# Performance work log

Hardware: AMD Instinct MI355X
Metric: run time of the kernel (lower is better)

## Reference

```python
import jax, jax.numpy as jnp
import numpy as np

# ---- module hyperparameters (match init_kwargs) ----
N_BASIS = 4            # lagrange polynomial order n
SEGMENTS = 32
IN_CHANNELS = 64
LENGTH = 2.0
HALF = 0.5 * LENGTH
W_WIDTH = (N_BASIS - 1) * SEGMENTS + 1  # 97
# Lagrange interpolation nodes on [-HALF, HALF] (uniform, as in high_order_layers_torch LagrangePoly)
_XNODES = np.linspace(-HALF, HALF, N_BASIS).astype(np.float32)


def _lagrange_basis(x):
    """x: [...] -> basis values [..., n]; basis_j(x) = prod_{m!=j} (x-X_m)/(X_j-X_m)."""
    X = jnp.asarray(_XNODES, dtype=x.dtype)
    eye = jnp.eye(N_BASIS, dtype=bool)
    denom = jnp.where(eye, 1.0, X[:, None] - X[None, :])          # [n, n]
    num = x[..., None, None] - X                                   # [..., 1, n] broadcast over j
    terms = jnp.where(eye, 1.0, num / denom)                       # [..., j, m]
    return jnp.prod(terms, axis=-1)                                # [..., n]


def setup_inputs() -> dict:
    key = jax.random.key(0)
    k1, k2 = jax.random.split(key)
    x = jax.random.normal(k1, (32, IN_CHANNELS, 4096), dtype=jnp.float32)
    w = jax.random.uniform(k2, (IN_CHANNELS, W_WIDTH), dtype=jnp.float32,
                           minval=-1.0, maxval=1.0)
    return {"x": x, "w": w}


def reference(x, w):
    B, C, N = x.shape  # [batch, channels, nodes]
    n = N_BASIS

    # bin index with torch-style trunc + clamp
    id_raw = jnp.trunc((x + HALF) / LENGTH * SEGMENTS).astype(jnp.int32)
    id_min = jnp.clip(id_raw, 0, SEGMENTS - 1)                     # [B, C, N]
    id_max = id_min + 1

    wid_min = id_min * (n - 1)                                     # [B, C, N]

    # gather n consecutive weights per element from the shared table
    E = B * C * N
    wrange = wid_min.reshape(-1)[:, None] + jnp.arange(n)          # [E, n]
    # original: windex = (arange(E*n)//n) % in_channels  == (arange(E) % C) per row
    windex = (jnp.arange(E) % C)[:, None]                          # [E, 1]
    wg = w[windex, wrange]                                         # [E, n]
    # original reshape: view(-1, nodes, in_channels, n)
    wv = wg.reshape(B, N, C, n)                                    # [B, N, C, n]

    # rescale x into the local segment coordinate [-HALF, HALF]
    eta = lambda idx: idx.astype(x.dtype) / SEGMENTS * 2.0 - 1.0
    x_min = eta(id_min)
    x_max = eta(id_max)
    x_in = LENGTH * ((x - x_min) / (x_max - x_min)) - HALF         # [B, C, N]

    basis = _lagrange_basis(x_in)                                  # [B, C, N, n]
    # contract basis with gathered weights (note transposed node/channel layout of wv)
    out = jnp.einsum("bcnj,bncj->bcn", basis, wv)                  # [B, C, N]
    return out
```

## Files before the change

kernel.cpp:

```cpp
#include <hip/hip_runtime.h>

#define NBATCH   32
#define NCH      64
#define NNODE    4096
#define WW       97
#define NTHREADS 512

typedef float     f32x4 __attribute__((ext_vector_type(4)));
typedef float     f32x2 __attribute__((ext_vector_type(2)));
typedef _Float16  h16x4 __attribute__((ext_vector_type(4)));

__global__ __launch_bounds__(NTHREADS)
void pw_kernel(const float* __restrict__ x,
               const float* __restrict__ w,
               float* __restrict__ out) {
  __shared__ h16x4 wexp[NCH * 32];

  const int g   = blockIdx.x;
  const int b   = (g & 7) | ((g >> 9) << 3);
  const int t   = (g >> 3) & 63;
  const int tid = threadIdx.x;

  #pragma unroll
  for (int k = 0; k < 4; ++k) {
    const int r = tid + k * NTHREADS;
    const int c = r >> 5, i = r & 31;
    const float* wr = w + c * WW + 3 * i;
    const float v0 = wr[0] * (-9.0f / 16.0f);
    const float v1 = wr[1] * (27.0f / 16.0f);
    const float v2 = wr[2] * (-27.0f / 16.0f);
    const float v3 = wr[3] * (9.0f / 16.0f);
    const float a3 = v0 + v1 + v2 + v3;
    const float a2 = -v0 - v1 * (1.0f / 3.0f) + v2 * (1.0f / 3.0f) + v3;
    const float a1 = -v0 * (1.0f / 9.0f) - v1 - v2 - v3 * (1.0f / 9.0f);
    const float a0 =  v0 * (1.0f / 9.0f) + v1 * (1.0f / 3.0f)
                    - v2 * (1.0f / 3.0f) - v3 * (1.0f / 9.0f);
    h16x4 h;
    h[0] = (_Float16)a0; h[1] = (_Float16)a1;
    h[2] = (_Float16)a2; h[3] = (_Float16)a3;
    wexp[r] = h;
  }
  __syncthreads();

  const int l  = tid & 63;
  const int wv = tid >> 6;
  const int q  = l & 15;
  const int a  = l >> 4;
  const int u0 = q << 2;
  const int c0 = (wv << 3) + (a << 1);

  const float* xrow = x + (((size_t)(b * NCH + t)) << 12);

  f32x2 src[4];
  #pragma unroll
  for (int i = 0; i < 4; ++i)
    src[i] = *reinterpret_cast<const f32x2*>(xrow + ((u0 + i) << 6) + c0);

  const size_t obase = (((size_t)(b * NCH + c0)) << 12) + ((size_t)(t << 6)) + u0;

  #pragma unroll
  for (int j = 0; j < 2; ++j) {
    const f32x4 own = *reinterpret_cast<const f32x4*>(x + obase + ((size_t)j << 12));
    const int cb = (c0 + j) << 5;
    f32x4 res;
    #pragma unroll
    for (int i = 0; i < 4; ++i) {
      const float xv = own[i];
      const float tt = fmaf(xv, 16.0f, 16.0f);
      int idm = (int)tt;
      idm = idm < 0 ? 0 : (idm > 31 ? 31 : idm);
      const float xin = fmaf(xv, 32.0f, fmaf((float)idm, -2.0f, 31.0f));

      const float sv = src[i][j];
      const float st = fmaf(sv, 16.0f, 16.0f);
      int idw = (int)st;
      idw = idw < 0 ? 0 : (idw > 31 ? 31 : idw);
      const h16x4 hc = wexp[cb + idw];

      const float c0f = (float)hc[0], c1f = (float)hc[1];
      const float c2f = (float)hc[2], c3f = (float)hc[3];
      res[i] = fmaf(fmaf(fmaf(c3f, xin, c2f), xin, c1f), xin, c0f);
    }
    __builtin_nontemporal_store(res,
        reinterpret_cast<f32x4*>(out + obase + ((size_t)j << 12)));
  }
}

extern "C" void kernel_launch(void* const* d_in, const int* in_sizes, int n_in,
                              void* d_out, int out_size, void* d_ws, size_t ws_size,
                              hipStream_t stream) {
  const float* x = (const float*)d_in[0];
  const float* w = (const float*)d_in[1];
  float* out    = (float*)d_out;
  pw_kernel<<<dim3(NBATCH * (NNODE / 64)), NTHREADS, 0, stream>>>(x, w, out);
}
```

Measured before the change: 20.34 us.

## Tile 3-index cyclic permutation orbits so each x value is read once

Reorganizes the work so that, per batch, each block handles an orbit of 16x16x16 tiles under the cyclic permutation of the (channel, tile, offset) index triple. The gathered weight index for one element comes from another element of the same orbit, so the kernel computes segment ids once, packs them as bytes into shared memory and reads them back instead of loading x twice. The grid drops to 24x32 blocks of 256 threads, with each block building the full weight-coefficient table again (8 rows per thread). It also replaces nontemporal stores with plain stores. The risks are fewer and heavier blocks with uneven work (orbits of size 1 versus 3), extra shared memory, and a larger share of time spent on the repeated table setup.

```diff
diff --git a/kernel.cpp b/kernel.cpp
--- a/kernel.cpp
+++ b/kernel.cpp
@@ -1,29 +1,40 @@
 #include <hip/hip_runtime.h>
 
-#define NBATCH   32
-#define NCH      64
-#define NNODE    4096
-#define WW       97
-#define NTHREADS 512
+#define NCH 64
+#define WW  97
 
-typedef float     f32x4 __attribute__((ext_vector_type(4)));
-typedef float     f32x2 __attribute__((ext_vector_type(2)));
-typedef _Float16  h16x4 __attribute__((ext_vector_type(4)));
+typedef float        f32x4 __attribute__((ext_vector_type(4)));
+typedef unsigned int u32x4v __attribute__((ext_vector_type(4)));
+typedef _Float16     h16x4 __attribute__((ext_vector_type(4)));
+typedef unsigned int u32;
 
-__global__ __launch_bounds__(NTHREADS)
+__constant__ unsigned char ORBITS[24] = {
+  0x00, 0x15, 0x2A, 0x3F,
+  0x01, 0x02, 0x03, 0x05, 0x0A, 0x0F,
+  0x06, 0x09, 0x07, 0x0D, 0x0B, 0x0E,
+  0x16, 0x17, 0x1A, 0x1F, 0x2B, 0x2F,
+  0x1B, 0x1E
+};
+
+__global__ __launch_bounds__(256)
 void pw_kernel(const float* __restrict__ x,
                const float* __restrict__ w,
                float* __restrict__ out) {
   __shared__ h16x4 wexp[NCH * 32];
+  __shared__ __align__(16) unsigned char sid[3][16 * 272];
 
-  const int g   = blockIdx.x;
-  const int b   = (g & 7) | ((g >> 9) << 3);
-  const int t   = (g >> 3) & 63;
+  const int b    = blockIdx.y;
+  const int ob   = ORBITS[blockIdx.x];
+  const int nreg = (blockIdx.x < 4) ? 1 : 3;
+  const int e0 = ((ob >> 4) & 3) << 4;
+  const int e1 = ((ob >> 2) & 3) << 4;
+  const int e2 = (ob & 3) << 4;
   const int tid = threadIdx.x;
+  const int rho = tid >> 4, sig = tid & 15;
 
   #pragma unroll
-  for (int k = 0; k < 4; ++k) {
-    const int r = tid + k * NTHREADS;
+  for (int kk = 0; kk < 8; ++kk) {
+    const int r = tid + (kk << 8);
     const int c = r >> 5, i = r & 31;
     const float* wr = w + c * WW + 3 * i;
     const float v0 = wr[0] * (-9.0f / 16.0f);
@@ -40,49 +51,73 @@
     h[2] = (_Float16)a2; h[3] = (_Float16)a3;
     wexp[r] = h;
   }
+
+  float vals[3][16];
+  #pragma unroll
+  for (int r = 0; r < 3; ++r) {
+    if (r < nreg) {
+      const int rowb = (r == 0) ? e0 : (r == 1) ? e1 : e2;
+      const int tilb = (r == 0) ? e1 : (r == 1) ? e2 : e0;
+      const int offb = (r == 0) ? e2 : (r == 1) ? e0 : e1;
+      const float* p = x + (((size_t)(b * NCH + rowb + rho)) << 12)
+                         + ((tilb + sig) << 6) + offb;
+      u32 pk[4];
+      #pragma unroll
+      for (int m = 0; m < 4; ++m) {
+        const f32x4 q = *reinterpret_cast<const f32x4*>(p + (m << 2));
+        u32 pw = 0;
+        #pragma unroll
+        for (int i = 0; i < 4; ++i) {
+          const float vv = q[i];
+          vals[r][m * 4 + i] = vv;
+          const float tt = fmaf(vv, 16.0f, 16.0f);
+          int id = (int)tt;
+          id = id < 0 ? 0 : (id > 31 ? 31 : id);
+          pw |= (u32)id << (8 * i);
+        }
+        pk[m] = pw;
+      }
+      u32x4v pv; pv[0] = pk[0]; pv[1] = pk[1]; pv[2] = pk[2]; pv[3] = pk[3];
+      *reinterpret_cast<u32x4v*>(&sid[r][rho * 272 + sig * 16]) = pv;
+    }
+  }
   __syncthreads();
 
-  const int l  = tid & 63;
-  const int wv = tid >> 6;
-  const int q  = l & 15;
-  const int a  = l >> 4;
-  const int u0 = q << 2;
-  const int c0 = (wv << 3) + (a << 1);
+  #pragma unroll
+  for (int n = 0; n < 3; ++n) {
+    if (n < nreg) {
+      const int cb = (n == 0) ? e0 : (n == 1) ? e1 : e2;
+      const int tb = (n == 0) ? e1 : (n == 1) ? e2 : e0;
+      const int ub = (n == 0) ? e2 : (n == 1) ? e0 : e1;
+      const int m  = (nreg == 1) ? 0 : (n + 1) % 3;
+      const int c  = cb + rho;
+      const int t  = tb + sig;
+      const u32* sp = reinterpret_cast<const u32*>(
+          &sid[m][sig * 272 + (rho & ~3)]);
+      const int sh = (rho & 3) * 8;
+      const int cw = c << 5;
+      float* op = out + (((size_t)(b * NCH + c)) << 12) + (t << 6) + ub;
 
-  const float* xrow = x + (((size_t)(b * NCH + t)) << 12);
+      #pragma unroll
+      for (int m4 = 0; m4 < 4; ++m4) {
+        f32x4 res;
+        #pragma unroll
+        for (int i = 0; i < 4; ++i) {
+          const int k = m4 * 4 + i;
+          const float xv = vals[n][k];
+          const float tt = fmaf(xv, 16.0f, 16.0f);
+          int idm = (int)tt;
+          idm = idm < 0 ? 0 : (idm > 31 ? 31 : idm);
+          const float xin = fmaf(xv, 32.0f, fmaf((float)idm, -2.0f, 31.0f));
 
-  f32x2 src[4];
-  #pragma unroll
-  for (int i = 0; i < 4; ++i)
-    src[i] = *reinterpret_cast<const f32x2*>(xrow + ((u0 + i) << 6) + c0);
-
-  const size_t obase = (((size_t)(b * NCH + c0)) << 12) + ((size_t)(t << 6)) + u0;
-
-  #pragma unroll
-  for (int j = 0; j < 2; ++j) {
-    const f32x4 own = *reinterpret_cast<const f32x4*>(x + obase + ((size_t)j << 12));
-    const int cb = (c0 + j) << 5;
-    f32x4 res;
-    #pragma unroll
-    for (int i = 0; i < 4; ++i) {
-      const float xv = own[i];
-      const float tt = fmaf(xv, 16.0f, 16.0f);
-      int idm = (int)tt;
-      idm = idm < 0 ? 0 : (idm > 31 ? 31 : idm);
-      const float xin = fmaf(xv, 32.0f, fmaf((float)idm, -2.0f, 31.0f));
-
-      const float sv = src[i][j];
-      const float st = fmaf(sv, 16.0f, 16.0f);
-      int idw = (int)st;
-      idw = idw < 0 ? 0 : (idw > 31 ? 31 : idw);
-      const h16x4 hc = wexp[cb + idw];
-
-      const float c0f = (float)hc[0], c1f = (float)hc[1];
-      const float c2f = (float)hc[2], c3f = (float)hc[3];
-      res[i] = fmaf(fmaf(fmaf(c3f, xin, c2f), xin, c1f), xin, c0f);
+          const int idw = (sp[k << 2] >> sh) & 31;
+          const h16x4 hc = wexp[cw + idw];
+          res[i] = fmaf(fmaf(fmaf((float)hc[3], xin, (float)hc[2]), xin,
+                             (float)hc[1]), xin, (float)hc[0]);
+        }
+        *reinterpret_cast<f32x4*>(op + (m4 << 2)) = res;
+      }
     }
-    __builtin_nontemporal_store(res,
-        reinterpret_cast<f32x4*>(out + obase + ((size_t)j << 12)));
   }
 }
 
@@ -92,5 +127,5 @@
   const float* x = (const float*)d_in[0];
   const float* w = (const float*)d_in[1];
   float* out    = (float*)d_out;
-  pw_kernel<<<dim3(NBATCH * (NNODE / 64)), NTHREADS, 0, stream>>>(x, w, out);
+  pw_kernel<<<dim3(24, 32), 256, 0, stream>>>(x, w, out);
 }
```

After: 26.95 us. 1.33x slower.
